# Kernel optimization log

Measured on AMD Instinct MI355X. Metric: run time of the kernel, lower is better.

Reference implementation:

```python
import jax, jax.numpy as jnp
import numpy as np

EPS = 1e-4

def softmax_kernel(data, proj, is_query):
    # FAVOR+ positive softmax random features; data: [b,h,l,d], proj: [d,m]
    d = data.shape[-1]
    m = proj.shape[-1]
    data_normalizer = d ** -0.25  # normalize_data=True
    ratio = m ** -0.5
    data_dash = jnp.einsum('bhld,dm->bhlm', data, proj) * data_normalizer
    diag = 0.5 * jnp.sum(data * data, axis=-1, keepdims=True) * (data_normalizer ** 2)
    if is_query:
        stab = jnp.max(data_dash, axis=-1, keepdims=True)   # per-token max
    else:
        stab = jnp.max(data_dash, axis=(-2, -1), keepdims=True)  # per (b,h) max
    out = ratio * (jnp.exp(data_dash - diag - stab) + EPS)
    return out, stab

def low_mem_attn(qp, kp, v, causal, chunk):
    # qp,kp: [b,h,l,m] positive features; v: [b,h,l,d]
    b, h, l, m = qp.shape
    d = v.shape[-1]
    if not causal:
        kv = jnp.einsum('bhlm,bhld->bhmd', kp, v)
        den = jnp.einsum('bhlm,bhm->bhl', qp, jnp.sum(kp, axis=2))
        return jnp.einsum('bhlm,bhmd->bhld', qp, kv) / den[..., None]
    nc = l // chunk
    qc = qp.reshape(b, h, nc, chunk, m)
    kc = kp.reshape(b, h, nc, chunk, m)
    vc = v.reshape(b, h, nc, chunk, d)
    # intra-chunk causal part
    mask = jnp.tril(jnp.ones((chunk, chunk), dtype=qp.dtype))
    scores = jnp.einsum('bhcim,bhcjm->bhcij', qc, kc) * mask
    intra = jnp.einsum('bhcij,bhcjd->bhcid', scores, vc)
    intra_den = jnp.sum(scores, axis=-1)  # [b,h,nc,chunk]
    # inter-chunk via exclusive cumulative sums of KV state
    kv = jnp.einsum('bhcjm,bhcjd->bhcmd', kc, vc)          # per-chunk KV
    kv_prev = jnp.cumsum(kv, axis=2) - kv                   # exclusive cumsum
    ks = jnp.sum(kc, axis=3)                                # [b,h,nc,m]
    ks_prev = jnp.cumsum(ks, axis=2) - ks
    inter = jnp.einsum('bhcim,bhcmd->bhcid', qc, kv_prev)
    inter_den = jnp.einsum('bhcim,bhcm->bhci', qc, ks_prev)
    out = (intra + inter) / (intra_den + inter_den)[..., None]
    return out.reshape(b, h, l, d)


def setup_inputs() -> dict:
    key = jax.random.key(0)
    k1, k2, k3, k4 = jax.random.split(key, 4)
    B, H, L, D, M = 2, 16, 4096, 64, 64
    return {
        'q': jax.random.normal(k1, (B, H, L, D), dtype=jnp.float32),
        'k': jax.random.normal(k2, (B, H, L, D), dtype=jnp.float32),
        'v': jax.random.normal(k3, (B, H, L, D), dtype=jnp.float32),
        'projection_matrix': jax.random.normal(k4, (D, M), dtype=jnp.float32),
        'chunk_size': 128,
    }


def reference(q, k, v, projection_matrix, chunk_size):
    qp, _ = softmax_kernel(q, projection_matrix, is_query=True)
    kp, _key_maxima = softmax_kernel(k, projection_matrix, is_query=False)
    o = low_mem_attn(qp, kp, v, causal=True, chunk=chunk_size)
    return o
```

## Files before the change

kernel.cpp:

```cpp
#include <hip/hip_runtime.h>
#include <hip/hip_bf16.h>

#define TPB 256
#define ATPB 512

constexpr int   Bc = 2, Hc = 16, Lc = 4096, Dc = 64, Mc = 64, CHc = 128;
constexpr int   NCc = Lc / CHc;
constexpr int   BHc = Bc * Hc;
constexpr float DNF    = 0.35355339059327373f;
constexpr float RATIOF = 0.125f;
constexpr float EPSF   = 1e-4f;

constexpr long QP_OFF  = 0;
constexpr long KP_OFF  = 4194304;
constexpr long KV_OFF  = 12582912;
constexpr long KVB_OFF = 16777216;
constexpr long KS_OFF  = 18874368;
constexpr long HM_OFF  = 18939904;

typedef __attribute__((ext_vector_type(8))) short bf16x8;
typedef __attribute__((ext_vector_type(4))) float f32x4;

__device__ __forceinline__ unsigned fordmap(float f) {
  unsigned u = __float_as_uint(f);
  return (u & 0x80000000u) ? ~u : (u | 0x80000000u);
}
__device__ __forceinline__ float fordunmap(unsigned u) {
  return __uint_as_float((u & 0x80000000u) ? (u & 0x7fffffffu) : ~u);
}
__device__ __forceinline__ unsigned pk2(float a, float b) {
  union { __hip_bfloat16 h; unsigned short u; } ca, cb;
  ca.h = __float2bfloat16(a); cb.h = __float2bfloat16(b);
  return ((unsigned)cb.u << 16) | (unsigned)ca.u;
}
__device__ __forceinline__ short f2bf(float a) {
  union { __hip_bfloat16 h; short s; } c; c.h = __float2bfloat16(a); return c.s;
}
__device__ __forceinline__ float bf2f(short s) {
  return __uint_as_float(((unsigned)(unsigned short)s) << 16);
}

__global__ void k_init(unsigned* hmax) {
  int t = threadIdx.x;
  if (t < BHc) hmax[t] = 0u;
}

template <bool IS_Q>
__global__ __launch_bounds__(TPB) void k_feat(const float* __restrict__ x,
                                              const float* __restrict__ P,
                                              float* __restrict__ outf,
                                              short* __restrict__ outb,
                                              unsigned* __restrict__ hmax) {
  __shared__ float xs[128 * 68];
  __shared__ float Ps[64 * 64];
  __shared__ float diag_s[128];
  __shared__ unsigned bmax_s;
  const int t = threadIdx.x;
  const long rowbase = (long)blockIdx.x * 128;
  for (int i = t; i < 128 * 64; i += TPB) {
    int r = i >> 6, d = i & 63;
    xs[r * 68 + d] = x[rowbase * 64 + i];
  }
  for (int i = t; i < 64 * 64; i += TPB) Ps[i] = P[i];
  if (t == 0) bmax_s = 0u;
  __syncthreads();
  if (t < 128) {
    float s = 0.f;
#pragma unroll
    for (int d = 0; d < 64; d += 4) {
      float4 vv = *(const float4*)&xs[t * 68 + d];
      s += vv.x * vv.x + vv.y * vv.y + vv.z * vv.z + vv.w * vv.w;
    }
    diag_s[t] = 0.0625f * s;
  }
  __syncthreads();
  const int g = t & 7, rg = t >> 3;
  const int m0 = g * 8, r0 = rg * 4;
  float acc[4][8];
#pragma unroll
  for (int r = 0; r < 4; ++r)
#pragma unroll
    for (int j = 0; j < 8; ++j) acc[r][j] = 0.f;
  for (int d0 = 0; d0 < 64; d0 += 4) {
    float4 xv[4];
#pragma unroll
    for (int r = 0; r < 4; ++r) xv[r] = *(const float4*)&xs[(r0 + r) * 68 + d0];
#pragma unroll
    for (int dq = 0; dq < 4; ++dq) {
      float4 p0 = *(const float4*)&Ps[(d0 + dq) * 64 + m0];
      float4 p1 = *(const float4*)&Ps[(d0 + dq) * 64 + m0 + 4];
#pragma unroll
      for (int r = 0; r < 4; ++r) {
        float xd = reinterpret_cast<const float*>(&xv[r])[dq];
        acc[r][0] += xd * p0.x; acc[r][1] += xd * p0.y;
        acc[r][2] += xd * p0.z; acc[r][3] += xd * p0.w;
        acc[r][4] += xd * p1.x; acc[r][5] += xd * p1.y;
        acc[r][6] += xd * p1.z; acc[r][7] += xd * p1.w;
      }
    }
  }
#pragma unroll
  for (int r = 0; r < 4; ++r)
#pragma unroll
    for (int j = 0; j < 8; ++j) acc[r][j] *= DNF;

  if constexpr (IS_Q) {
#pragma unroll
    for (int r = 0; r < 4; ++r) {
      float mx = acc[r][0];
#pragma unroll
      for (int j = 1; j < 8; ++j) mx = fmaxf(mx, acc[r][j]);
#pragma unroll
      for (int off = 1; off < 8; off <<= 1) mx = fmaxf(mx, __shfl_xor(mx, off));
      const float dg = diag_s[r0 + r];
      float o[8];
#pragma unroll
      for (int j = 0; j < 8; ++j) o[j] = RATIOF * (expf(acc[r][j] - dg - mx) + EPSF);
      uint4 ov;
      ov.x = pk2(o[0], o[1]); ov.y = pk2(o[2], o[3]);
      ov.z = pk2(o[4], o[5]); ov.w = pk2(o[6], o[7]);
      *(uint4*)&outb[(rowbase + r0 + r) * 64 + m0] = ov;
    }
  } else {
    float tmax = acc[0][0];
#pragma unroll
    for (int r = 0; r < 4; ++r)
#pragma unroll
      for (int j = 0; j < 8; ++j) tmax = fmaxf(tmax, acc[r][j]);
#pragma unroll
    for (int r = 0; r < 4; ++r) {
      const float dg = diag_s[r0 + r];
      float4 o0, o1;
      float* o0f = (float*)&o0; float* o1f = (float*)&o1;
#pragma unroll
      for (int j = 0; j < 4; ++j) o0f[j] = acc[r][j] - dg;
#pragma unroll
      for (int j = 0; j < 4; ++j) o1f[j] = acc[r][4 + j] - dg;
      const long ob = (rowbase + r0 + r) * 64 + m0;
      *(float4*)&outf[ob] = o0;
      *(float4*)&outf[ob + 4] = o1;
    }
    atomicMax(&bmax_s, fordmap(tmax));
    __syncthreads();
    if (t == 0) atomicMax(&hmax[rowbase >> 12], bmax_s);
  }
}

__global__ __launch_bounds__(TPB) void k_ckv(const float* __restrict__ kp,
                                             const float* __restrict__ v,
                                             float* __restrict__ kvT,
                                             float* __restrict__ ks,
                                             const unsigned* __restrict__ hmax) {
  __shared__ float kps[128 * 68];
  __shared__ float vs[128 * 68];
  const int t = threadIdx.x;
  const int bhc = blockIdx.x;
  const long base = (long)bhc * 8192;
  const float stab = fordunmap(hmax[bhc >> 5]);
  for (int i = t; i < 8192; i += TPB) {
    int r = i >> 6, d = i & 63;
    kps[r * 68 + d] = RATIOF * (expf(kp[base + i] - stab) + EPSF);
    vs[r * 68 + d]  = v[base + i];
  }
  __syncthreads();
  const int dd = t & 31, mg = t >> 5;
  const int d0 = dd * 2, m0 = mg * 8;
  float a0[8], a1[8];
#pragma unroll
  for (int i = 0; i < 8; ++i) { a0[i] = 0.f; a1[i] = 0.f; }
  for (int j = 0; j < 128; ++j) {
    float2 vv = *(const float2*)&vs[j * 68 + d0];
    float4 k0 = *(const float4*)&kps[j * 68 + m0];
    float4 k1 = *(const float4*)&kps[j * 68 + m0 + 4];
    a0[0] += vv.x * k0.x; a0[1] += vv.x * k0.y; a0[2] += vv.x * k0.z; a0[3] += vv.x * k0.w;
    a0[4] += vv.x * k1.x; a0[5] += vv.x * k1.y; a0[6] += vv.x * k1.z; a0[7] += vv.x * k1.w;
    a1[0] += vv.y * k0.x; a1[1] += vv.y * k0.y; a1[2] += vv.y * k0.z; a1[3] += vv.y * k0.w;
    a1[4] += vv.y * k1.x; a1[5] += vv.y * k1.y; a1[6] += vv.y * k1.z; a1[7] += vv.y * k1.w;
  }
  const long kvb = (long)bhc * 4096;
  *(float4*)&kvT[kvb + (long)d0 * 64 + m0]           = make_float4(a0[0], a0[1], a0[2], a0[3]);
  *(float4*)&kvT[kvb + (long)d0 * 64 + m0 + 4]       = make_float4(a0[4], a0[5], a0[6], a0[7]);
  *(float4*)&kvT[kvb + (long)(d0 + 1) * 64 + m0]     = make_float4(a1[0], a1[1], a1[2], a1[3]);
  *(float4*)&kvT[kvb + (long)(d0 + 1) * 64 + m0 + 4] = make_float4(a1[4], a1[5], a1[6], a1[7]);
  if (t < 64) {
    float s = 0.f;
    for (int j = 0; j < 128; ++j) s += kps[j * 68 + t];
    ks[bhc * 64 + t] = s;
  }
}

__global__ void k_scan_kv(const float* __restrict__ kv, short* __restrict__ kvb) {
  const int tid = blockIdx.x * TPB + threadIdx.x;
  const int bh = tid >> 12, rem = tid & 4095;
  float run = 0.f;
  for (int c = 0; c < NCc; ++c) {
    const long idx = ((long)(bh * NCc + c)) * 4096 + rem;
    kvb[idx] = f2bf(run);
    run += kv[idx];
  }
}

__global__ void k_scan_ks(float* __restrict__ ks) {
  const int tid = blockIdx.x * TPB + threadIdx.x;
  if (tid >= BHc * 64) return;
  const int bh = tid >> 6, m = tid & 63;
  float run = 0.f;
  for (int c = 0; c < NCc; ++c) {
    const int idx = (bh * NCc + c) * 64 + m;
    const float val = ks[idx];
    ks[idx] = run;
    run += val;
  }
}

__global__ __launch_bounds__(ATPB, 4) void k_attn(const short* __restrict__ qpb,
                                                  const float* __restrict__ kp,
                                                  const float* __restrict__ v,
                                                  const short* __restrict__ kvb,
                                                  const float* __restrict__ ksp,
                                                  const unsigned* __restrict__ hmax,
                                                  float* __restrict__ outp) {
  __shared__ short Ks[128 * 72];
  __shared__ short Vt[64 * 136];
  __shared__ short KVt[64 * 72];
  __shared__ short Ps[128 * 136];
  __shared__ float kss[64];
  __shared__ float dens[128];
  const int t = threadIdx.x;
  const int bhc = blockIdx.x;
  const long cbase = (long)bhc * 8192;
  const float stab = fordunmap(hmax[bhc >> 5]);

  for (int i = t; i < 4096; i += ATPB) {
    const int r = i >> 5, d2 = (i & 31) * 2;
    float2 kk = *(const float2*)&kp[cbase + r * 64 + d2];
    const float e0 = RATIOF * (expf(kk.x - stab) + EPSF);
    const float e1 = RATIOF * (expf(kk.y - stab) + EPSF);
    *(unsigned*)&Ks[r * 72 + d2] = pk2(e0, e1);
  }
  for (int i = t; i < 4096; i += ATPB) {
    const int jp = i >> 6, d = i & 63;
    const float a = v[cbase + (2 * jp) * 64 + d];
    const float b = v[cbase + (2 * jp + 1) * 64 + d];
    *(unsigned*)&Vt[d * 136 + 2 * jp] = pk2(a, b);
  }
  {
    const int d = t >> 3, c8 = (t & 7) * 8;
    *(uint4*)&KVt[d * 72 + c8] = *(const uint4*)&kvb[(long)bhc * 4096 + d * 64 + c8];
  }
  if (t < 64) kss[t] = ksp[bhc * 64 + t];
  for (int i = t; i < 1024; i += ATPB) {
    const int tp = i >> 8, rr = (i >> 4) & 15, cc = i & 15;
    Ps[(tp * 32 + rr) * 136 + tp * 32 + 16 + cc] = 0;
  }
  const int w = t >> 6, lane = t & 63;
  const int lrow = lane & 15, quad = lane >> 4;
  const int ri = w;
  const long qrb = cbase + (long)(ri * 16 + lrow) * 64;
  const bf16x8 a0 = *(const bf16x8*)&qpb[qrb + quad * 8];
  const bf16x8 a1 = *(const bf16x8*)&qpb[qrb + 32 + quad * 8];
  __syncthreads();

  float qks = 0.f;
#pragma unroll
  for (int j = 0; j < 8; ++j) {
    qks += bf2f(a0[j]) * kss[quad * 8 + j];
    qks += bf2f(a1[j]) * kss[32 + quad * 8 + j];
  }
  qks += __shfl_xor(qks, 16);
  qks += __shfl_xor(qks, 32);
  if (quad == 0) dens[ri * 16 + lrow] = qks;

  float rs0 = 0.f, rs1 = 0.f, rs2 = 0.f, rs3 = 0.f;
  for (int cj = 0; cj <= ri; ++cj) {
    const bf16x8 b0 = *(const bf16x8*)&Ks[(cj * 16 + lrow) * 72 + quad * 8];
    const bf16x8 b1 = *(const bf16x8*)&Ks[(cj * 16 + lrow) * 72 + 32 + quad * 8];
    f32x4 c = {0.f, 0.f, 0.f, 0.f};
    c = __builtin_amdgcn_mfma_f32_16x16x32_bf16(a0, b0, c, 0, 0, 0);
    c = __builtin_amdgcn_mfma_f32_16x16x32_bf16(a1, b1, c, 0, 0, 0);
    if (cj == ri) {
#pragma unroll
      for (int r = 0; r < 4; ++r)
        if (lrow > quad * 4 + r) c[r] = 0.f;
    }
    const int colb = cj * 16 + lrow;
    Ps[(ri * 16 + quad * 4 + 0) * 136 + colb] = f2bf(c[0]); rs0 += c[0];
    Ps[(ri * 16 + quad * 4 + 1) * 136 + colb] = f2bf(c[1]); rs1 += c[1];
    Ps[(ri * 16 + quad * 4 + 2) * 136 + colb] = f2bf(c[2]); rs2 += c[2];
    Ps[(ri * 16 + quad * 4 + 3) * 136 + colb] = f2bf(c[3]); rs3 += c[3];
  }
#pragma unroll
  for (int off = 1; off < 16; off <<= 1) {
    rs0 += __shfl_xor(rs0, off);
    rs1 += __shfl_xor(rs1, off);
    rs2 += __shfl_xor(rs2, off);
    rs3 += __shfl_xor(rs3, off);
  }
  if (lrow == 0) {
    dens[ri * 16 + quad * 4 + 0] += rs0;
    dens[ri * 16 + quad * 4 + 1] += rs1;
    dens[ri * 16 + quad * 4 + 2] += rs2;
    dens[ri * 16 + quad * 4 + 3] += rs3;
  }

  f32x4 acc0 = {0.f,0.f,0.f,0.f}, acc1 = {0.f,0.f,0.f,0.f};
  f32x4 acc2 = {0.f,0.f,0.f,0.f}, acc3 = {0.f,0.f,0.f,0.f};
  const int nj = (ri + 2) >> 1;
  for (int jc = 0; jc < nj; ++jc) {
    const bf16x8 a  = *(const bf16x8*)&Ps[(ri * 16 + lrow) * 136 + jc * 32 + quad * 8];
    const bf16x8 b0 = *(const bf16x8*)&Vt[(lrow) * 136 + jc * 32 + quad * 8];
    const bf16x8 b1 = *(const bf16x8*)&Vt[(16 + lrow) * 136 + jc * 32 + quad * 8];
    const bf16x8 b2 = *(const bf16x8*)&Vt[(32 + lrow) * 136 + jc * 32 + quad * 8];
    const bf16x8 b3 = *(const bf16x8*)&Vt[(48 + lrow) * 136 + jc * 32 + quad * 8];
    acc0 = __builtin_amdgcn_mfma_f32_16x16x32_bf16(a, b0, acc0, 0, 0, 0);
    acc1 = __builtin_amdgcn_mfma_f32_16x16x32_bf16(a, b1, acc1, 0, 0, 0);
    acc2 = __builtin_amdgcn_mfma_f32_16x16x32_bf16(a, b2, acc2, 0, 0, 0);
    acc3 = __builtin_amdgcn_mfma_f32_16x16x32_bf16(a, b3, acc3, 0, 0, 0);
  }
  {
    const bf16x8 b0 = *(const bf16x8*)&KVt[(lrow) * 72 + quad * 8];
    const bf16x8 b1 = *(const bf16x8*)&KVt[(16 + lrow) * 72 + quad * 8];
    const bf16x8 b2 = *(const bf16x8*)&KVt[(32 + lrow) * 72 + quad * 8];
    const bf16x8 b3 = *(const bf16x8*)&KVt[(48 + lrow) * 72 + quad * 8];
    acc0 = __builtin_amdgcn_mfma_f32_16x16x32_bf16(a0, b0, acc0, 0, 0, 0);
    acc1 = __builtin_amdgcn_mfma_f32_16x16x32_bf16(a0, b1, acc1, 0, 0, 0);
    acc2 = __builtin_amdgcn_mfma_f32_16x16x32_bf16(a0, b2, acc2, 0, 0, 0);
    acc3 = __builtin_amdgcn_mfma_f32_16x16x32_bf16(a0, b3, acc3, 0, 0, 0);
    const bf16x8 c0 = *(const bf16x8*)&KVt[(lrow) * 72 + 32 + quad * 8];
    const bf16x8 c1 = *(const bf16x8*)&KVt[(16 + lrow) * 72 + 32 + quad * 8];
    const bf16x8 c2 = *(const bf16x8*)&KVt[(32 + lrow) * 72 + 32 + quad * 8];
    const bf16x8 c3 = *(const bf16x8*)&KVt[(48 + lrow) * 72 + 32 + quad * 8];
    acc0 = __builtin_amdgcn_mfma_f32_16x16x32_bf16(a1, c0, acc0, 0, 0, 0);
    acc1 = __builtin_amdgcn_mfma_f32_16x16x32_bf16(a1, c1, acc1, 0, 0, 0);
    acc2 = __builtin_amdgcn_mfma_f32_16x16x32_bf16(a1, c2, acc2, 0, 0, 0);
    acc3 = __builtin_amdgcn_mfma_f32_16x16x32_bf16(a1, c3, acc3, 0, 0, 0);
  }
#pragma unroll
  for (int r = 0; r < 4; ++r) {
    const int row = ri * 16 + quad * 4 + r;
    const float inv = 1.f / dens[row];
    const long ob = cbase + (long)row * 64 + lrow;
    outp[ob]      = acc0[r] * inv;
    outp[ob + 16] = acc1[r] * inv;
    outp[ob + 32] = acc2[r] * inv;
    outp[ob + 48] = acc3[r] * inv;
  }
}

extern "C" void kernel_launch(void* const* d_in, const int* in_sizes, int n_in,
                              void* d_out, int out_size, void* d_ws, size_t ws_size,
                              hipStream_t stream) {
  const float* q = (const float*)d_in[0];
  const float* k = (const float*)d_in[1];
  const float* v = (const float*)d_in[2];
  const float* P = (const float*)d_in[3];
  float* ws = (float*)d_ws;
  short*    qpb  = (short*)(ws + QP_OFF);
  float*    kp   = ws + KP_OFF;
  float*    kvT  = ws + KV_OFF;
  short*    kvb  = (short*)(ws + KVB_OFF);
  float*    ks   = ws + KS_OFF;
  unsigned* hmax = (unsigned*)(ws + HM_OFF);
  float* out = (float*)d_out;

  k_init<<<1, 64, 0, stream>>>(hmax);
  k_feat<true><<<dim3(1024), dim3(TPB), 0, stream>>>(q, P, nullptr, qpb, nullptr);
  k_feat<false><<<dim3(1024), dim3(TPB), 0, stream>>>(k, P, kp, nullptr, hmax);
  k_ckv<<<dim3(1024), dim3(TPB), 0, stream>>>(kp, v, kvT, ks, hmax);
  k_scan_kv<<<dim3(512), dim3(TPB), 0, stream>>>(kvT, kvb);
  k_scan_ks<<<dim3(8), dim3(TPB), 0, stream>>>(ks);
  k_attn<<<dim3(1024), dim3(ATPB), 0, stream>>>(qpb, kp, v, kvb, ks, hmax, out);
}
```

Measured before the change: 233.9 us.

## Use bf16 MFMA for feature projection and precompute bf16 K/V tiles for attention

The feature kernel now does the x·P projection with bf16 MFMA instructions, staging results in shared memory before writing them out coalesced, instead of scalar fp32 FMAs. The chunk-KV kernel also writes bf16 copies of the exponentiated key features and a transposed bf16 V, so the attention kernel loads ready-made tiles instead of recomputing exp and repacking fp32 data. This removes duplicated exp work and halves the bytes the attention kernel loads, at the cost of extra workspace writes and lower precision in the projection.

```diff
diff --git a/kernel.cpp b/kernel.cpp
--- a/kernel.cpp
+++ b/kernel.cpp
@@ -13,10 +13,12 @@
 
 constexpr long QP_OFF  = 0;
 constexpr long KP_OFF  = 4194304;
-constexpr long KV_OFF  = 12582912;
-constexpr long KVB_OFF = 16777216;
-constexpr long KS_OFF  = 18874368;
-constexpr long HM_OFF  = 18939904;
+constexpr long KPB_OFF = 12582912;
+constexpr long VTB_OFF = 16777216;
+constexpr long KV_OFF  = 20971520;
+constexpr long KVB_OFF = 25165824;
+constexpr long KS_OFF  = 27262976;
+constexpr long HM_OFF  = 27328512;
 
 typedef __attribute__((ext_vector_type(8))) short bf16x8;
 typedef __attribute__((ext_vector_type(4))) float f32x4;
@@ -51,97 +53,98 @@
                                               float* __restrict__ outf,
                                               short* __restrict__ outb,
                                               unsigned* __restrict__ hmax) {
-  __shared__ float xs[128 * 68];
-  __shared__ float Ps[64 * 64];
+  __shared__ short xb[128 * 72];
+  __shared__ short Pt[64 * 72];
+  __shared__ float od[128 * 68];
   __shared__ float diag_s[128];
   __shared__ unsigned bmax_s;
   const int t = threadIdx.x;
   const long rowbase = (long)blockIdx.x * 128;
-  for (int i = t; i < 128 * 64; i += TPB) {
-    int r = i >> 6, d = i & 63;
-    xs[r * 68 + d] = x[rowbase * 64 + i];
-  }
-  for (int i = t; i < 64 * 64; i += TPB) Ps[i] = P[i];
+  for (int i = t; i < 4096; i += TPB) {
+    const int r = i >> 5, d2 = (i & 31) * 2;
+    float2 xv = *(const float2*)&x[rowbase * 64 + r * 64 + d2];
+    *(unsigned*)&xb[r * 72 + d2] = pk2(xv.x, xv.y);
+  }
+  for (int i = t; i < 4096; i += TPB) {
+    const int d = i >> 6, m = i & 63;
+    Pt[m * 72 + d] = f2bf(P[i]);
+  }
   if (t == 0) bmax_s = 0u;
+  {
+    const int row = t >> 1, half = t & 1;
+    float s = 0.f;
+#pragma unroll
+    for (int d = 0; d < 32; d += 4) {
+      float4 vv = *(const float4*)&x[(rowbase + row) * 64 + half * 32 + d];
+      s += vv.x * vv.x + vv.y * vv.y + vv.z * vv.z + vv.w * vv.w;
+    }
+    s += __shfl_xor(s, 1);
+    if (half == 0) diag_s[row] = 0.0625f * s;
+  }
   __syncthreads();
-  if (t < 128) {
-    float s = 0.f;
-#pragma unroll
-    for (int d = 0; d < 64; d += 4) {
-      float4 vv = *(const float4*)&xs[t * 68 + d];
-      s += vv.x * vv.x + vv.y * vv.y + vv.z * vv.z + vv.w * vv.w;
-    }
-    diag_s[t] = 0.0625f * s;
+
+  const int w = t >> 6, lane = t & 63;
+  const int lrow = lane & 15, quad = lane >> 4;
+  float tmax = -1e30f;
+#pragma unroll
+  for (int rt2 = 0; rt2 < 2; ++rt2) {
+    const int rt = w * 2 + rt2;
+    const bf16x8 a0 = *(const bf16x8*)&xb[(rt * 16 + lrow) * 72 + quad * 8];
+    const bf16x8 a1 = *(const bf16x8*)&xb[(rt * 16 + lrow) * 72 + 32 + quad * 8];
+    f32x4 c[4];
+#pragma unroll
+    for (int ct = 0; ct < 4; ++ct) {
+      const bf16x8 b0 = *(const bf16x8*)&Pt[(ct * 16 + lrow) * 72 + quad * 8];
+      const bf16x8 b1 = *(const bf16x8*)&Pt[(ct * 16 + lrow) * 72 + 32 + quad * 8];
+      f32x4 cc = {0.f, 0.f, 0.f, 0.f};
+      cc = __builtin_amdgcn_mfma_f32_16x16x32_bf16(a0, b0, cc, 0, 0, 0);
+      cc = __builtin_amdgcn_mfma_f32_16x16x32_bf16(a1, b1, cc, 0, 0, 0);
+#pragma unroll
+      for (int r = 0; r < 4; ++r) cc[r] *= DNF;
+      c[ct] = cc;
+    }
+    if constexpr (IS_Q) {
+      short* ob = (short*)od;
+#pragma unroll
+      for (int r = 0; r < 4; ++r) {
+        float mx = fmaxf(fmaxf(c[0][r], c[1][r]), fmaxf(c[2][r], c[3][r]));
+#pragma unroll
+        for (int off = 1; off < 16; off <<= 1) mx = fmaxf(mx, __shfl_xor(mx, off));
+        const int row = rt * 16 + quad * 4 + r;
+        const float dg = diag_s[row];
+#pragma unroll
+        for (int ct = 0; ct < 4; ++ct)
+          ob[row * 64 + ct * 16 + lrow] =
+              f2bf(RATIOF * (expf(c[ct][r] - dg - mx) + EPSF));
+      }
+    } else {
+#pragma unroll
+      for (int r = 0; r < 4; ++r) {
+        const int row = rt * 16 + quad * 4 + r;
+        const float dg = diag_s[row];
+#pragma unroll
+        for (int ct = 0; ct < 4; ++ct) {
+          tmax = fmaxf(tmax, c[ct][r]);
+          od[row * 68 + ct * 16 + lrow] = c[ct][r] - dg;
+        }
+      }
+    }
+  }
+  if constexpr (!IS_Q) {
+#pragma unroll
+    for (int off = 1; off < 64; off <<= 1) tmax = fmaxf(tmax, __shfl_xor(tmax, off));
+    if (lane == 0) atomicMax(&bmax_s, fordmap(tmax));
   }
   __syncthreads();
-  const int g = t & 7, rg = t >> 3;
-  const int m0 = g * 8, r0 = rg * 4;
-  float acc[4][8];
-#pragma unroll
-  for (int r = 0; r < 4; ++r)
-#pragma unroll
-    for (int j = 0; j < 8; ++j) acc[r][j] = 0.f;
-  for (int d0 = 0; d0 < 64; d0 += 4) {
-    float4 xv[4];
-#pragma unroll
-    for (int r = 0; r < 4; ++r) xv[r] = *(const float4*)&xs[(r0 + r) * 68 + d0];
-#pragma unroll
-    for (int dq = 0; dq < 4; ++dq) {
-      float4 p0 = *(const float4*)&Ps[(d0 + dq) * 64 + m0];
-      float4 p1 = *(const float4*)&Ps[(d0 + dq) * 64 + m0 + 4];
-#pragma unroll
-      for (int r = 0; r < 4; ++r) {
-        float xd = reinterpret_cast<const float*>(&xv[r])[dq];
-        acc[r][0] += xd * p0.x; acc[r][1] += xd * p0.y;
-        acc[r][2] += xd * p0.z; acc[r][3] += xd * p0.w;
-        acc[r][4] += xd * p1.x; acc[r][5] += xd * p1.y;
-        acc[r][6] += xd * p1.z; acc[r][7] += xd * p1.w;
-      }
-    }
-  }
-#pragma unroll
-  for (int r = 0; r < 4; ++r)
-#pragma unroll
-    for (int j = 0; j < 8; ++j) acc[r][j] *= DNF;
-
   if constexpr (IS_Q) {
-#pragma unroll
-    for (int r = 0; r < 4; ++r) {
-      float mx = acc[r][0];
-#pragma unroll
-      for (int j = 1; j < 8; ++j) mx = fmaxf(mx, acc[r][j]);
-#pragma unroll
-      for (int off = 1; off < 8; off <<= 1) mx = fmaxf(mx, __shfl_xor(mx, off));
-      const float dg = diag_s[r0 + r];
-      float o[8];
-#pragma unroll
-      for (int j = 0; j < 8; ++j) o[j] = RATIOF * (expf(acc[r][j] - dg - mx) + EPSF);
-      uint4 ov;
-      ov.x = pk2(o[0], o[1]); ov.y = pk2(o[2], o[3]);
-      ov.z = pk2(o[4], o[5]); ov.w = pk2(o[6], o[7]);
-      *(uint4*)&outb[(rowbase + r0 + r) * 64 + m0] = ov;
-    }
+    const short* ob = (const short*)od;
+    for (int i = t; i < 1024; i += TPB)
+      *(uint4*)&outb[rowbase * 64 + i * 8] = *(const uint4*)&ob[i * 8];
   } else {
-    float tmax = acc[0][0];
-#pragma unroll
-    for (int r = 0; r < 4; ++r)
-#pragma unroll
-      for (int j = 0; j < 8; ++j) tmax = fmaxf(tmax, acc[r][j]);
-#pragma unroll
-    for (int r = 0; r < 4; ++r) {
-      const float dg = diag_s[r0 + r];
-      float4 o0, o1;
-      float* o0f = (float*)&o0; float* o1f = (float*)&o1;
-#pragma unroll
-      for (int j = 0; j < 4; ++j) o0f[j] = acc[r][j] - dg;
-#pragma unroll
-      for (int j = 0; j < 4; ++j) o1f[j] = acc[r][4 + j] - dg;
-      const long ob = (rowbase + r0 + r) * 64 + m0;
-      *(float4*)&outf[ob] = o0;
-      *(float4*)&outf[ob + 4] = o1;
-    }
-    atomicMax(&bmax_s, fordmap(tmax));
-    __syncthreads();
+    for (int i = t; i < 2048; i += TPB) {
+      const int row = i >> 4, c4 = (i & 15) * 4;
+      *(float4*)&outf[rowbase * 64 + row * 64 + c4] = *(const float4*)&od[row * 68 + c4];
+    }
     if (t == 0) atomicMax(&hmax[rowbase >> 12], bmax_s);
   }
 }
@@ -150,6 +153,8 @@
                                              const float* __restrict__ v,
                                              float* __restrict__ kvT,
                                              float* __restrict__ ks,
+                                             short* __restrict__ kpb,
+                                             short* __restrict__ vtb,
                                              const unsigned* __restrict__ hmax) {
   __shared__ float kps[128 * 68];
   __shared__ float vs[128 * 68];
@@ -163,6 +168,17 @@
     vs[r * 68 + d]  = v[base + i];
   }
   __syncthreads();
+  for (int i = t; i < 2048; i += TPB) {
+    const int r = i >> 4, c4 = (i & 15) * 4;
+    float4 kk = *(const float4*)&kps[r * 68 + c4];
+    uint2 pk; pk.x = pk2(kk.x, kk.y); pk.y = pk2(kk.z, kk.w);
+    *(uint2*)&kpb[base + r * 64 + c4] = pk;
+  }
+  for (int i = t; i < 4096; i += TPB) {
+    const int jp = i & 63, d = i >> 6;
+    *(unsigned*)&vtb[base + d * 128 + 2 * jp] =
+        pk2(vs[(2 * jp) * 68 + d], vs[(2 * jp + 1) * 68 + d]);
+  }
   const int dd = t & 31, mg = t >> 5;
   const int d0 = dd * 2, m0 = mg * 8;
   float a0[8], a1[8];
@@ -214,11 +230,10 @@
 }
 
 __global__ __launch_bounds__(ATPB, 4) void k_attn(const short* __restrict__ qpb,
-                                                  const float* __restrict__ kp,
-                                                  const float* __restrict__ v,
+                                                  const short* __restrict__ kpb,
+                                                  const short* __restrict__ vtb,
                                                   const short* __restrict__ kvb,
                                                   const float* __restrict__ ksp,
-                                                  const unsigned* __restrict__ hmax,
                                                   float* __restrict__ outp) {
   __shared__ short Ks[128 * 72];
   __shared__ short Vt[64 * 136];
@@ -229,20 +244,14 @@
   const int t = threadIdx.x;
   const int bhc = blockIdx.x;
   const long cbase = (long)bhc * 8192;
-  const float stab = fordunmap(hmax[bhc >> 5]);
-
-  for (int i = t; i < 4096; i += ATPB) {
-    const int r = i >> 5, d2 = (i & 31) * 2;
-    float2 kk = *(const float2*)&kp[cbase + r * 64 + d2];
-    const float e0 = RATIOF * (expf(kk.x - stab) + EPSF);
-    const float e1 = RATIOF * (expf(kk.y - stab) + EPSF);
-    *(unsigned*)&Ks[r * 72 + d2] = pk2(e0, e1);
-  }
-  for (int i = t; i < 4096; i += ATPB) {
-    const int jp = i >> 6, d = i & 63;
-    const float a = v[cbase + (2 * jp) * 64 + d];
-    const float b = v[cbase + (2 * jp + 1) * 64 + d];
-    *(unsigned*)&Vt[d * 136 + 2 * jp] = pk2(a, b);
+
+  for (int i = t; i < 1024; i += ATPB) {
+    const int r = i >> 3, c8 = (i & 7) * 8;
+    *(uint4*)&Ks[r * 72 + c8] = *(const uint4*)&kpb[cbase + r * 64 + c8];
+  }
+  for (int i = t; i < 1024; i += ATPB) {
+    const int d = i >> 4, c8 = (i & 15) * 8;
+    *(uint4*)&Vt[d * 136 + c8] = *(const uint4*)&vtb[cbase + d * 128 + c8];
   }
   {
     const int d = t >> 3, c8 = (t & 7) * 8;
@@ -357,6 +366,8 @@
   float* ws = (float*)d_ws;
   short*    qpb  = (short*)(ws + QP_OFF);
   float*    kp   = ws + KP_OFF;
+  short*    kpb  = (short*)(ws + KPB_OFF);
+  short*    vtb  = (short*)(ws + VTB_OFF);
   float*    kvT  = ws + KV_OFF;
   short*    kvb  = (short*)(ws + KVB_OFF);
   float*    ks   = ws + KS_OFF;
@@ -366,8 +377,8 @@
   k_init<<<1, 64, 0, stream>>>(hmax);
   k_feat<true><<<dim3(1024), dim3(TPB), 0, stream>>>(q, P, nullptr, qpb, nullptr);
   k_feat<false><<<dim3(1024), dim3(TPB), 0, stream>>>(k, P, kp, nullptr, hmax);
-  k_ckv<<<dim3(1024), dim3(TPB), 0, stream>>>(kp, v, kvT, ks, hmax);
+  k_ckv<<<dim3(1024), dim3(TPB), 0, stream>>>(kp, v, kvT, ks, kpb, vtb, hmax);
   k_scan_kv<<<dim3(512), dim3(TPB), 0, stream>>>(kvT, kvb);
   k_scan_ks<<<dim3(8), dim3(TPB), 0, stream>>>(ks);
-  k_attn<<<dim3(1024), dim3(ATPB), 0, stream>>>(qpb, kp, v, kvb, ks, hmax, out);
-}
+  k_attn<<<dim3(1024), dim3(ATPB), 0, stream>>>(qpb, kpb, vtb, kvb, ks, out);
+}
```

After: 224.9 us. 3.8% less time.
